# Performance work log

Measured on AMD Instinct MI355X. Metric: run time of the kernel, lower is better.

The kernel has to match this reference:

```python
import jax, jax.numpy as jnp
import numpy as np

B, L, D = 2, 2048, 2048
H, KVH, Dh = 16, 8, 128
S_ROPE = 1024
EPS = 1e-5


def rms_norm(x, w):
    xf = x.astype(jnp.float32)
    xf = xf * jax.lax.rsqrt(jnp.mean(xf * xf, axis=-1, keepdims=True) + EPS)
    return (xf * w).astype(x.dtype)


def rotate_half(x):
    x1, x2 = jnp.split(x, 2, axis=-1)
    return jnp.concatenate((-x2, x1), axis=-1)


def setup_inputs() -> dict:
    key = jax.random.key(0)
    ks = jax.random.split(key, 12)
    sc = 0.02
    # 1D rope tables at every absolute position (theta = 500000 as in config)
    inv_freq = 1.0 / (500000.0 ** (np.arange(0, Dh, 2, dtype=np.float32) / Dh))
    ang = np.arange(L, dtype=np.float32)[:, None] * inv_freq[None, :]  # [L, Dh/2]
    emb = np.concatenate([ang, ang], axis=-1)  # [L, Dh]
    # 3D rope as per-pair 2x2 rotation matrices
    ang3 = np.random.RandomState(0).uniform(-np.pi, np.pi, size=(S_ROPE, Dh // 2)).astype(np.float32)
    R = np.stack([np.stack([np.cos(ang3), -np.sin(ang3)], -1),
                  np.stack([np.sin(ang3), np.cos(ang3)], -1)], -2)  # [S,Dh/2,2,2]
    mpos = jnp.array([[[128, 1025], [1160, 513]],
                      [[128, 1025], [1160, 513]]], dtype=jnp.int64)
    return {
        "hidden_states": jax.random.normal(ks[0], (B, L, D), jnp.float32),
        "temb": jax.random.normal(ks[1], (B, D), jnp.float32),
        "w_ln": jnp.ones((D,), jnp.float32),
        "w_mod": jax.random.normal(ks[2], (D, 3 * D), jnp.float32) * sc,
        "b_mod": jnp.zeros((3 * D,), jnp.float32),
        "wq": jax.random.normal(ks[3], (D, H * Dh), jnp.float32) * sc,
        "wk": jax.random.normal(ks[4], (D, KVH * Dh), jnp.float32) * sc,
        "wv": jax.random.normal(ks[5], (D, KVH * Dh), jnp.float32) * sc,
        "wo": jax.random.normal(ks[6], (H * Dh, D), jnp.float32) * sc,
        "qn_w": jnp.ones((Dh,), jnp.float32),
        "kn_w": jnp.ones((Dh,), jnp.float32),
        "cos_1d": jnp.asarray(np.cos(emb)),
        "sin_1d": jnp.asarray(np.sin(emb)),
        "rope_3d": jnp.asarray(R),
        "modality_positions": mpos,
    }


def _masks(modality_positions):
    pos = jnp.arange(L)  # [L]
    off = modality_positions[..., 0]   # [B, S]
    ln = modality_positions[..., 1]    # [B, S]
    meta = 1  # add_time_embeds=True, add_ar_embeds=False
    seg_end = off + jnp.maximum(ln, meta)
    in_full = (pos[None, None, :] >= off[..., None]) & (pos[None, None, :] < seg_end[..., None])
    text_mask = ~jnp.any(in_full, axis=1)  # [B, L]
    img_start = off + meta
    in_img = (pos[None, None, :] >= img_start[..., None]) & (pos[None, None, :] < (off + ln)[..., None])
    rel = jnp.sum(jnp.where(in_img, pos[None, None, :] - img_start[..., None], 0), axis=1)  # [B, L]
    img_mask = jnp.any(in_img, axis=1) & (rel < S_ROPE) & (rel >= 0)
    rel = jnp.clip(rel, 0, S_ROPE - 1)
    return text_mask, img_mask, rel


def _apply_mixed_rope(q, k, cos_1d, sin_1d, rope_3d, text_mask, img_mask, rel):
    # text 1D rope (rotate_half style), applied at absolute position
    c = cos_1d[None, None]  # [1,1,L,Dh]
    s = sin_1d[None, None]
    q_txt = q * c + rotate_half(q) * s
    k_txt = k * c + rotate_half(k) * s
    # image 3D rope: per-pair 2x2 rotation gathered at within-image index
    R = rope_3d[rel]  # [B, L, Dh/2, 2, 2]
    q2 = q.reshape(*q.shape[:-1], Dh // 2, 2)
    k2 = k.reshape(*k.shape[:-1], Dh // 2, 2)
    q_img = jnp.einsum('bhlpi,blpij->bhlpj', q2, R).reshape(q.shape)
    k_img = jnp.einsum('bhlpi,blpij->bhlpj', k2, R).reshape(k.shape)
    mt = text_mask[:, None, :, None]
    mi = img_mask[:, None, :, None]
    q_out = jnp.where(mt, q_txt, jnp.where(mi, q_img, q))
    k_out = jnp.where(mt, k_txt, jnp.where(mi, k_img, k))
    return q_out, k_out


def reference(hidden_states, temb, w_ln, w_mod, b_mod, wq, wk, wv, wo,
              qn_w, kn_w, cos_1d, sin_1d, rope_3d, modality_positions):
    dtype = hidden_states.dtype
    # adaLN modulation
    mod = jax.nn.silu(temb) @ w_mod + b_mod  # [B, 3D]
    shift, scale, gate = jnp.split(mod, 3, axis=-1)
    xn = rms_norm(hidden_states, w_ln)
    xm = (xn.astype(jnp.float32) * (1.0 + scale[:, None, :].astype(jnp.float32))
          + shift[:, None, :].astype(jnp.float32)).astype(dtype)
    # qkv projections (GQA)
    q = (xm @ wq).reshape(B, L, H, Dh).transpose(0, 2, 1, 3)
    k = (xm @ wk).reshape(B, L, KVH, Dh).transpose(0, 2, 1, 3)
    v = (xm @ wv).reshape(B, L, KVH, Dh).transpose(0, 2, 1, 3)
    # qk-norm over head_dim
    q = rms_norm(q, qn_w)
    k = rms_norm(k, kn_w)
    # mixed 3D-image / 1D-text RoPE
    text_mask, img_mask, rel = _masks(modality_positions)
    q, k = _apply_mixed_rope(q, k, cos_1d, sin_1d, rope_3d, text_mask, img_mask, rel)
    # GQA: repeat kv heads (repeat_interleave along head dim)
    n_rep = H // KVH
    k = jnp.repeat(k, n_rep, axis=1)
    v = jnp.repeat(v, n_rep, axis=1)
    # full attention (no causal mask for diffusion block)
    scores = jnp.einsum('bhqd,bhkd->bhqk', q, k) / jnp.sqrt(jnp.asarray(Dh, q.dtype))
    attn = jax.nn.softmax(scores, axis=-1)
    o = jnp.einsum('bhqk,bhkd->bhqd', attn, v)
    o = o.transpose(0, 2, 1, 3).reshape(B, L, H * Dh) @ wo
    return hidden_states + gate[:, None, :].astype(dtype) * o


if __name__ == '__main__':
    out = reference(**setup_inputs())
    print(out.shape, out.dtype)
```

## Files before the change

kernel.cpp:

```cpp
#include <hip/hip_runtime.h>
#include <stdint.h>
#include <math.h>

typedef unsigned short u16;
typedef __attribute__((ext_vector_type(8))) short short8;
typedef __attribute__((ext_vector_type(4))) float fx4;
typedef __attribute__((ext_vector_type(4))) unsigned short u16x4;

#define DEV __device__ __forceinline__

DEV u16 f2bf(float f) {
  unsigned u = __builtin_bit_cast(unsigned, f);
  return (u16)((u + 0x7FFFu + ((u >> 16) & 1u)) >> 16);
}
DEV float bf2f(u16 h) { return __builtin_bit_cast(float, ((unsigned)h) << 16); }

DEV fx4 mfma16(short8 a, short8 b, fx4 c) {
  return __builtin_amdgcn_mfma_f32_16x16x32_bf16(a, b, c, 0, 0, 0);
}

#if __has_builtin(__builtin_amdgcn_exp2f)
DEV float exp2v(float x) { return __builtin_amdgcn_exp2f(x); }
#else
DEV float exp2v(float x) { return exp2f(x); }
#endif

#define GLD16(g, l)                                                            \
  __builtin_amdgcn_global_load_lds(                                            \
      (const __attribute__((address_space(1))) void*)(g),                      \
      (__attribute__((address_space(3))) void*)(l), 16, 0, 0)

#define WAIT_ALL() asm volatile("s_waitcnt vmcnt(0) lgkmcnt(0)" ::: "memory")

__global__ __launch_bounds__(512) void k_silu_mod(
    const float* __restrict__ temb, const float* __restrict__ wmod,
    const float* __restrict__ bmod, float* __restrict__ mod) {
  __shared__ float st[4096];
  __shared__ float red[8][2][64];
  int tid = threadIdx.x;
  for (int i = tid; i < 4096; i += 512) {
    float t = temb[i];
    st[i] = t / (1.0f + __expf(-t));
  }
  __syncthreads();
  int j = blockIdx.x * 64 + (tid & 63);
  int ks = tid >> 6;
  float a0 = 0.f, a1 = 0.f;
  for (int d = ks * 256; d < ks * 256 + 256; ++d) {
    float w = wmod[(size_t)d * 6144 + j];
    a0 += st[d] * w;
    a1 += st[2048 + d] * w;
  }
  red[ks][0][tid & 63] = a0;
  red[ks][1][tid & 63] = a1;
  __syncthreads();
  if (tid < 64) {
    float s0 = 0.f, s1 = 0.f;
#pragma unroll
    for (int i = 0; i < 8; ++i) {
      s0 += red[i][0][tid];
      s1 += red[i][1][tid];
    }
    mod[j] = s0 + bmod[j];
    mod[6144 + j] = s1 + bmod[j];
  }
}

__global__ __launch_bounds__(256) void k_xm(
    const float* __restrict__ x, const float* __restrict__ wln,
    const float* __restrict__ mod, u16* __restrict__ xm) {
  int row = blockIdx.x;
  int b = row >> 11;
  const float* xr = x + (size_t)row * 2048;
  int tid = threadIdx.x;
  float4 v0 = ((const float4*)xr)[tid];
  float4 v1 = ((const float4*)xr)[tid + 256];
  float ss = v0.x * v0.x + v0.y * v0.y + v0.z * v0.z + v0.w * v0.w +
             v1.x * v1.x + v1.y * v1.y + v1.z * v1.z + v1.w * v1.w;
  for (int m = 1; m < 64; m <<= 1) ss += __shfl_xor(ss, m);
  __shared__ float red[4];
  if ((tid & 63) == 0) red[tid >> 6] = ss;
  __syncthreads();
  ss = red[0] + red[1] + red[2] + red[3];
  float r = rsqrtf(ss * (1.0f / 2048.0f) + 1e-5f);
  const float* mb = mod + (size_t)b * 6144;
#pragma unroll
  for (int c = 0; c < 2; ++c) {
    int j0 = (tid + c * 256) * 4;
    float4 xv = c ? v1 : v0;
    float4 sh = *(const float4*)(mb + j0);
    float4 sc = *(const float4*)(mb + 2048 + j0);
    float4 wl = *(const float4*)(wln + j0);
    u16x4 o;
    o.x = f2bf(xv.x * r * wl.x * (1.f + sc.x) + sh.x);
    o.y = f2bf(xv.y * r * wl.y * (1.f + sc.y) + sh.y);
    o.z = f2bf(xv.z * r * wl.z * (1.f + sc.z) + sh.z);
    o.w = f2bf(xv.w * r * wl.w * (1.f + sc.w) + sh.w);
    *(u16x4*)(xm + (size_t)row * 2048 + j0) = o;
  }
}

__global__ __launch_bounds__(256) void k_tconv(
    const float* __restrict__ src, u16* __restrict__ dst, int cols, int rows) {
  __shared__ float t[32][33];
  int kb = blockIdx.x * 32, nb = blockIdx.y * 32;
  int tx = threadIdx.x, ty = threadIdx.y;
#pragma unroll
  for (int i = 0; i < 4; ++i)
    t[ty + i * 8][tx] = src[(size_t)(kb + ty + i * 8) * cols + nb + tx];
  __syncthreads();
#pragma unroll
  for (int i = 0; i < 4; ++i)
    dst[(size_t)(nb + ty + i * 8) * rows + kb + tx] = f2bf(t[tx][ty + i * 8]);
}

template <int EPI>
__global__ __launch_bounds__(256) void k_gemm(
    const u16* __restrict__ A, const u16* __restrict__ Bt, void* __restrict__ Cp,
    const float* __restrict__ hid, const float* __restrict__ mod, int N, int K) {
  __shared__ u16 As[2][128 * 32];
  __shared__ u16 Bs[2][128 * 32];
  int tid = threadIdx.x;
  int wave = tid >> 6, lane = tid & 63, quad = lane >> 4, l16 = lane & 15;
  int gx = gridDim.x;
  int nwg = gx * gridDim.y;
  int lin = blockIdx.y * gx + blockIdx.x;
  int cpx = nwg >> 3;
  int swz = (lin & 7) * cpx + (lin >> 3);
  int m0 = (swz / gx) * 128, n0 = (swz % gx) * 128;
  int wm = (wave >> 1) * 64, wn = (wave & 1) * 64;
  fx4 acc[4][4] = {};
  int rowa = tid >> 2;
  int chunk = (tid & 3) ^ ((rowa >> 1) & 3);
  int cola = chunk * 8;
  const u16* Ag = A + (size_t)(m0 + rowa) * K + cola;
  const u16* Bg = Bt + (size_t)(n0 + rowa) * K + cola;
  int sl = (quad ^ ((l16 >> 1) & 3)) * 8;

  auto STAGE = [&](int k0, int buf) {
    u16* AsW = &As[buf][wave * 512];
    u16* BsW = &Bs[buf][wave * 512];
    GLD16(Ag + k0, AsW);
    GLD16(Ag + k0 + (size_t)64 * K, AsW + 2048);
    GLD16(Bg + k0, BsW);
    GLD16(Bg + k0 + (size_t)64 * K, BsW + 2048);
  };
  auto COMPUTE = [&](int buf) {
    short8 af[4], bfr[4];
#pragma unroll
    for (int i = 0; i < 4; ++i) {
      af[i] = *(const short8*)&As[buf][(wm + i * 16 + l16) * 32 + sl];
      bfr[i] = *(const short8*)&Bs[buf][(wn + i * 16 + l16) * 32 + sl];
    }
#pragma unroll
    for (int i = 0; i < 4; ++i)
#pragma unroll
      for (int j = 0; j < 4; ++j) acc[i][j] = mfma16(af[i], bfr[j], acc[i][j]);
  };

  STAGE(0, 0);
  WAIT_ALL();
  __builtin_amdgcn_s_barrier();
  int cur = 0;
  for (int k0 = 32; k0 < K; k0 += 32) {
    STAGE(k0, cur ^ 1);
    COMPUTE(cur);
    WAIT_ALL();
    __builtin_amdgcn_s_barrier();
    cur ^= 1;
  }
  COMPUTE(cur);

#pragma unroll
  for (int i = 0; i < 4; ++i) {
    int row = m0 + wm + i * 16 + quad * 4;
#pragma unroll
    for (int j = 0; j < 4; ++j) {
      int col = n0 + wn + j * 16 + l16;
      if (EPI == 0) {
        u16* C = (u16*)Cp;
#pragma unroll
        for (int r = 0; r < 4; ++r)
          C[(size_t)(row + r) * N + col] = f2bf(acc[i][j][r]);
      } else {
        float* C = (float*)Cp;
        int b = row >> 11;
        float g = mod[(size_t)b * 6144 + 4096 + col];
#pragma unroll
        for (int r = 0; r < 4; ++r)
          C[(size_t)(row + r) * N + col] =
              hid[(size_t)(row + r) * N + col] + g * acc[i][j][r];
      }
    }
  }
}

__global__ __launch_bounds__(192) void k_qknorm(
    const u16* __restrict__ qkv, const float* __restrict__ qn,
    const float* __restrict__ kn, const float* __restrict__ cos1,
    const float* __restrict__ sin1, const float* __restrict__ r3,
    const int* __restrict__ mpos, u16* __restrict__ Q, u16* __restrict__ Kb) {
  int bx = blockIdx.x;
  int b = bx >> 11, l = bx & 2047;
  int tid = threadIdx.x;
  int slot = tid >> 3, sub = tid & 7;
  bool isq = slot < 16;
  int head = isq ? slot : slot - 16;
  const u16* base = qkv + (size_t)bx * 4096 + (isq ? slot * 128 : 2048 + head * 128);
  int d0 = sub * 16;
  float xv[16];
#pragma unroll
  for (int i = 0; i < 16; ++i) xv[i] = bf2f(base[d0 + i]);
  float ss = 0.f;
#pragma unroll
  for (int i = 0; i < 16; ++i) ss += xv[i] * xv[i];
  ss += __shfl_xor(ss, 1);
  ss += __shfl_xor(ss, 2);
  ss += __shfl_xor(ss, 4);
  float r = rsqrtf(ss * (1.0f / 128.0f) + 1e-5f);
  int mp[8];
  {
    bool is64 = (mpos[1] == 0) & (mpos[3] == 0) & (mpos[5] == 0) & (mpos[7] == 0);
#pragma unroll
    for (int i = 0; i < 8; ++i) mp[i] = is64 ? mpos[2 * i] : mpos[i];
  }
  bool infull = false, inimg = false;
  int rel = 0;
#pragma unroll
  for (int s = 0; s < 2; ++s) {
    int off = mp[b * 4 + s * 2], ln = mp[b * 4 + s * 2 + 1];
    int mx = ln > 1 ? ln : 1;
    infull |= (l >= off) && (l < off + mx);
    bool ii = (l >= off + 1) && (l < off + ln);
    inimg |= ii;
    rel += ii ? (l - (off + 1)) : 0;
  }
  bool text = !infull;
  bool img = inimg && (rel < 1024);
  const float* w = isq ? qn : kn;
  float out[16];
  if (text) {
    int dp0 = d0 ^ 64;
    float sgn = (d0 < 64) ? -1.f : 1.f;
#pragma unroll
    for (int i = 0; i < 16; ++i) {
      int d = d0 + i, dp = dp0 + i;
      float c = cos1[(size_t)l * 128 + d];
      float s = sin1[(size_t)l * 128 + d];
      float xp = bf2f(base[dp]);
      out[i] = r * (xv[i] * w[d] * c + sgn * xp * w[dp] * s);
    }
  } else if (img) {
    const float* R = r3 + ((size_t)rel * 64 + (d0 >> 1)) * 4;
#pragma unroll
    for (int p = 0; p < 8; ++p) {
      float a = xv[2 * p] * w[d0 + 2 * p] * r;
      float c2 = xv[2 * p + 1] * w[d0 + 2 * p + 1] * r;
      out[2 * p] = a * R[4 * p + 0] + c2 * R[4 * p + 2];
      out[2 * p + 1] = a * R[4 * p + 1] + c2 * R[4 * p + 3];
    }
  } else {
#pragma unroll
    for (int i = 0; i < 16; ++i) out[i] = xv[i] * w[d0 + i] * r;
  }
  if (isq) {
    u16* dst = Q + ((size_t)(b * 16 + head) * 2048 + l) * 128 + d0;
#pragma unroll
    for (int i = 0; i < 16; ++i)
      dst[i] = f2bf(out[i] * (0.08838834764831845f * 1.4426950408889634f));
  } else {
    u16* dst = Kb + ((size_t)(b * 8 + head) * 2048 + l) * 128 + d0;
#pragma unroll
    for (int i = 0; i < 16; ++i) dst[i] = f2bf(out[i]);
  }
}

__global__ __launch_bounds__(256) void k_vtrans(const u16* __restrict__ qkv,
                                                u16* __restrict__ VT) {
  __shared__ u16 t[64][65];
  int bh = blockIdx.x;
  int l0 = blockIdx.y * 64, d0 = blockIdx.z * 64;
  int b = bh >> 3, kvh = bh & 7;
  int tx = threadIdx.x & 63, tg = threadIdx.x >> 6;
#pragma unroll
  for (int i = 0; i < 16; ++i) {
    int li = tg + i * 4;
    t[li][tx] = qkv[(size_t)(b * 2048 + l0 + li) * 4096 + 3072 + kvh * 128 + d0 + tx];
  }
  __syncthreads();
#pragma unroll
  for (int i = 0; i < 16; ++i) {
    int di = tg + i * 4;
    VT[((size_t)bh * 128 + d0 + di) * 2048 + l0 + tx] = t[tx][di];
  }
}

__global__ __launch_bounds__(512, 4) void k_attn(
    const u16* __restrict__ Q, const u16* __restrict__ Kb,
    const u16* __restrict__ VT, u16* __restrict__ O) {
  __shared__ u16 Ks[2][64 * 128];
  __shared__ u16 Vs[2][128 * 64];
  __shared__ u16 Ps[128 * 64];
  int tid = threadIdx.x;
  int wave = tid >> 6, lane = tid & 63, quad = lane >> 4, l16 = lane & 15;
  int bh = blockIdx.y;
  int b = bh >> 4, h = bh & 15, kvh = h >> 1;
  int q0 = blockIdx.x * 128;
  const u16* Qb = Q + ((size_t)bh * 2048 + q0 + wave * 16) * 128;
  short8 qf[4];
#pragma unroll
  for (int ks = 0; ks < 4; ++ks)
    qf[ks] = *(const short8*)(Qb + l16 * 128 + ks * 32 + quad * 8);
  const u16* Kg = Kb + (size_t)(b * 8 + kvh) * 2048 * 128;
  const u16* Vg = VT + (size_t)(b * 8 + kvh) * 128 * 2048;
  float mrow[4], lpart[4];
  fx4 of[8] = {};
#pragma unroll
  for (int r = 0; r < 4; ++r) {
    mrow[r] = -INFINITY;
    lpart[r] = 0.f;
  }
  size_t kgo[2], vgo[2];
#pragma unroll
  for (int i = 0; i < 2; ++i) {
    int kr = i * 32 + wave * 4 + (lane >> 4);
    kgo[i] = (size_t)kr * 128 + (((lane & 15) ^ (kr & 15)) * 8);
    int vr = i * 64 + wave * 8 + (lane >> 3);
    vgo[i] = (size_t)vr * 2048 + (((lane & 7) ^ (vr & 7)) * 8);
  }

  auto STAGE = [&](int t, int buf) {
    size_t ko = (size_t)t * 8192;
    size_t vo = (size_t)t * 64;
#pragma unroll
    for (int i = 0; i < 2; ++i) {
      GLD16(Kg + ko + kgo[i], &Ks[buf][i * 4096 + wave * 512]);
      GLD16(Vg + vo + vgo[i], &Vs[buf][i * 4096 + wave * 512]);
    }
  };

  auto COMPUTE = [&](int buf) {
    fx4 sf[4] = {};
    __builtin_amdgcn_s_setprio(1);
#pragma unroll
    for (int ct = 0; ct < 4; ++ct) {
#pragma unroll
      for (int ks = 0; ks < 4; ++ks) {
        short8 kf = *(const short8*)&Ks[buf][(ct * 16 + l16) * 128 +
                                            (((ks * 4 + quad) ^ l16) * 8)];
        sf[ct] = mfma16(qf[ks], kf, sf[ct]);
      }
    }
    __builtin_amdgcn_s_setprio(0);
    float cmv[4];
    bool need = false;
#pragma unroll
    for (int r = 0; r < 4; ++r) {
      cmv[r] = fmaxf(fmaxf(sf[0][r], sf[1][r]), fmaxf(sf[2][r], sf[3][r]));
      need |= (cmv[r] > mrow[r] + 8.0f);
    }
    if (__any(need)) {
#pragma unroll
      for (int r = 0; r < 4; ++r) {
        float cm = cmv[r];
        cm = fmaxf(cm, __shfl_xor(cm, 1));
        cm = fmaxf(cm, __shfl_xor(cm, 2));
        cm = fmaxf(cm, __shfl_xor(cm, 4));
        cm = fmaxf(cm, __shfl_xor(cm, 8));
        float mn = fmaxf(mrow[r], cm);
        float al = exp2v(mrow[r] - mn);
        mrow[r] = mn;
        lpart[r] *= al;
#pragma unroll
        for (int c2 = 0; c2 < 8; ++c2) of[c2][r] *= al;
      }
    }
    int hb = l16 >> 3;
#pragma unroll
    for (int r = 0; r < 4; ++r) {
      float p0 = exp2v(sf[0][r] - mrow[r]);
      float p1 = exp2v(sf[1][r] - mrow[r]);
      float p2 = exp2v(sf[2][r] - mrow[r]);
      float p3 = exp2v(sf[3][r] - mrow[r]);
      lpart[r] += (p0 + p1) + (p2 + p3);
      int prow = wave * 16 + quad * 4 + r;
      int pb = prow * 64, px = prow & 7, lo = l16 & 7;
      Ps[pb + ((0 + hb) ^ px) * 8 + lo] = f2bf(p0);
      Ps[pb + ((2 + hb) ^ px) * 8 + lo] = f2bf(p1);
      Ps[pb + ((4 + hb) ^ px) * 8 + lo] = f2bf(p2);
      Ps[pb + ((6 + hb) ^ px) * 8 + lo] = f2bf(p3);
    }
    __builtin_amdgcn_s_setprio(1);
#pragma unroll
    for (int ks2 = 0; ks2 < 2; ++ks2) {
      int rsl = (((ks2 * 4 + quad) ^ (l16 & 7)) * 8);
      short8 pa = *(const short8*)&Ps[(wave * 16 + l16) * 64 + rsl];
#pragma unroll
      for (int c2 = 0; c2 < 8; ++c2) {
        short8 vb = *(const short8*)&Vs[buf][(c2 * 16 + l16) * 64 + rsl];
        of[c2] = mfma16(pa, vb, of[c2]);
      }
    }
    __builtin_amdgcn_s_setprio(0);
  };

  STAGE(0, 0);
  WAIT_ALL();
  __builtin_amdgcn_s_barrier();
  int cur = 0;
  for (int t = 0; t < 31; ++t) {
    STAGE(t + 1, cur ^ 1);
    COMPUTE(cur);
    WAIT_ALL();
    __builtin_amdgcn_s_barrier();
    cur ^= 1;
  }
  COMPUTE(cur);

#pragma unroll
  for (int r = 0; r < 4; ++r) {
    float ls = lpart[r];
    ls += __shfl_xor(ls, 1);
    ls += __shfl_xor(ls, 2);
    ls += __shfl_xor(ls, 4);
    ls += __shfl_xor(ls, 8);
    float inv = 1.0f / ls;
    int qrow = q0 + wave * 16 + quad * 4 + r;
#pragma unroll
    for (int c2 = 0; c2 < 8; ++c2)
      O[((size_t)b * 2048 + qrow) * 2048 + h * 128 + c2 * 16 + l16] =
          f2bf(of[c2][r] * inv);
  }
}

extern "C" void kernel_launch(void* const* d_in, const int* in_sizes, int n_in,
                              void* d_out, int out_size, void* d_ws, size_t ws_size,
                              hipStream_t stream) {
  (void)in_sizes; (void)n_in; (void)out_size; (void)ws_size;
  const float* hid  = (const float*)d_in[0];
  const float* temb = (const float*)d_in[1];
  const float* wln  = (const float*)d_in[2];
  const float* wmod = (const float*)d_in[3];
  const float* bmod = (const float*)d_in[4];
  const float* wq   = (const float*)d_in[5];
  const float* wk   = (const float*)d_in[6];
  const float* wv   = (const float*)d_in[7];
  const float* wo   = (const float*)d_in[8];
  const float* qn   = (const float*)d_in[9];
  const float* kn   = (const float*)d_in[10];
  const float* cos1 = (const float*)d_in[11];
  const float* sin1 = (const float*)d_in[12];
  const float* r3   = (const float*)d_in[13];
  const int*   mpos = (const int*)d_in[14];

  char* ws = (char*)d_ws;
  float* mod = (float*)(ws + 0);
  u16* xm  = (u16*)(ws + 49152);
  u16* wT  = (u16*)(ws + 16826368);
  u16* woT = wT;
  u16* qkv = (u16*)(ws + 33603584);
  u16* Qb  = (u16*)(ws + 67158016);
  u16* Kv  = (u16*)(ws + 83935232);
  u16* VT  = (u16*)(ws + 92323840);
  u16* Ob  = qkv;

  dim3 b32(32, 8);
  k_silu_mod<<<96, 512, 0, stream>>>(temb, wmod, bmod, mod);
  k_tconv<<<dim3(64, 64), b32, 0, stream>>>(wq, wT, 2048, 2048);
  k_tconv<<<dim3(64, 32), b32, 0, stream>>>(wk, wT + (size_t)2048 * 2048, 1024, 2048);
  k_tconv<<<dim3(64, 32), b32, 0, stream>>>(wv, wT + (size_t)3072 * 2048, 1024, 2048);
  k_xm<<<4096, 256, 0, stream>>>(hid, wln, mod, xm);
  k_gemm<0><<<dim3(32, 32), 256, 0, stream>>>(xm, wT, qkv, nullptr, nullptr, 4096, 2048);
  k_tconv<<<dim3(64, 64), b32, 0, stream>>>(wo, woT, 2048, 2048);
  k_qknorm<<<4096, 192, 0, stream>>>(qkv, qn, kn, cos1, sin1, r3, mpos, Qb, Kv);
  k_vtrans<<<dim3(16, 32, 2), 256, 0, stream>>>(qkv, VT);
  k_attn<<<dim3(16, 32), 512, 0, stream>>>(Qb, Kv, VT, Ob);
  k_gemm<1><<<dim3(16, 32), 256, 0, stream>>>(Ob, woT, d_out, hid, mod, 2048, 2048);
}
```

Baseline: 487.4 us.

## Add 256x256 triple-buffered QKV GEMM and triple-buffer the output GEMM

Adds a dedicated QKV projection GEMM with 256x256 tiles, 512 threads, and a three-stage LDS ring. It waits with vmcnt(4) so one stage's loads stay in flight during compute, instead of draining everything every iteration. The output-projection GEMM gets the same three-buffer pipeline and becomes a single non-templated kernel. Larger tiles raise reuse per load, but the QKV launch is only 256 workgroups with one block per CU, and the extra LDS lowers occupancy.

Result: faster. 475.5 us (-2.4%).

```diff
diff --git a/kernel.cpp b/kernel.cpp
--- a/kernel.cpp
+++ b/kernel.cpp
@@ -31,6 +31,8 @@
       (__attribute__((address_space(3))) void*)(l), 16, 0, 0)
 
 #define WAIT_ALL() asm volatile("s_waitcnt vmcnt(0) lgkmcnt(0)" ::: "memory")
+#define WAIT_VM4() asm volatile("s_waitcnt vmcnt(4)" ::: "memory")
+#define WAIT_VM0() asm volatile("s_waitcnt vmcnt(0)" ::: "memory")
 
 __global__ __launch_bounds__(512) void k_silu_mod(
     const float* __restrict__ temb, const float* __restrict__ wmod,
@@ -114,12 +116,83 @@
     dst[(size_t)(nb + ty + i * 8) * rows + kb + tx] = f2bf(t[tx][ty + i * 8]);
 }
 
-template <int EPI>
+__global__ __launch_bounds__(512, 1) void k_gemm256(
+    const u16* __restrict__ A, const u16* __restrict__ Bt, u16* __restrict__ C,
+    int N, int K) {
+  __shared__ u16 As[3][256 * 32];
+  __shared__ u16 Bs[3][256 * 32];
+  int tid = threadIdx.x;
+  int wave = tid >> 6, lane = tid & 63, quad = lane >> 4, l16 = lane & 15;
+  int gx = gridDim.x;
+  int nwg = gx * gridDim.y;
+  int lin = blockIdx.y * gx + blockIdx.x;
+  int cpx = nwg >> 3;
+  int swz = (lin & 7) * cpx + (lin >> 3);
+  int m0 = (swz / gx) * 256, n0 = (swz % gx) * 256;
+  int wm = (wave >> 2) * 128, wn = (wave & 3) * 64;
+  fx4 acc[8][4] = {};
+  int rowa = tid >> 2;
+  int chunk = (tid & 3) ^ ((rowa >> 1) & 3);
+  int cola = chunk * 8;
+  const u16* Ag = A + (size_t)(m0 + rowa) * K + cola;
+  const u16* Bg = Bt + (size_t)(n0 + rowa) * K + cola;
+  int sl = (quad ^ ((l16 >> 1) & 3)) * 8;
+
+  auto STAGE = [&](int k0, int buf) {
+    u16* AsW = &As[buf][wave * 512];
+    u16* BsW = &Bs[buf][wave * 512];
+    GLD16(Ag + k0, AsW);
+    GLD16(Ag + k0 + (size_t)128 * K, AsW + 4096);
+    GLD16(Bg + k0, BsW);
+    GLD16(Bg + k0 + (size_t)128 * K, BsW + 4096);
+  };
+  auto COMPUTE = [&](int buf) {
+    short8 af[8], bfr[4];
+#pragma unroll
+    for (int i = 0; i < 8; ++i)
+      af[i] = *(const short8*)&As[buf][(wm + i * 16 + l16) * 32 + sl];
+#pragma unroll
+    for (int j = 0; j < 4; ++j)
+      bfr[j] = *(const short8*)&Bs[buf][(wn + j * 16 + l16) * 32 + sl];
+#pragma unroll
+    for (int i = 0; i < 8; ++i)
+#pragma unroll
+      for (int j = 0; j < 4; ++j) acc[i][j] = mfma16(af[i], bfr[j], acc[i][j]);
+  };
+
+  STAGE(0, 0);
+  STAGE(32, 1);
+  for (int t = 0; t < 62; ++t) {
+    WAIT_VM4();
+    __builtin_amdgcn_s_barrier();
+    STAGE((t + 2) * 32, (t + 2) % 3);
+    COMPUTE(t % 3);
+  }
+  WAIT_VM4();
+  __builtin_amdgcn_s_barrier();
+  COMPUTE(2);
+  WAIT_VM0();
+  __builtin_amdgcn_s_barrier();
+  COMPUTE(0);
+
+#pragma unroll
+  for (int i = 0; i < 8; ++i) {
+    int row = m0 + wm + i * 16 + quad * 4;
+#pragma unroll
+    for (int j = 0; j < 4; ++j) {
+      int col = n0 + wn + j * 16 + l16;
+#pragma unroll
+      for (int r = 0; r < 4; ++r)
+        C[(size_t)(row + r) * N + col] = f2bf(acc[i][j][r]);
+    }
+  }
+}
+
 __global__ __launch_bounds__(256) void k_gemm(
-    const u16* __restrict__ A, const u16* __restrict__ Bt, void* __restrict__ Cp,
+    const u16* __restrict__ A, const u16* __restrict__ Bt, float* __restrict__ C,
     const float* __restrict__ hid, const float* __restrict__ mod, int N, int K) {
-  __shared__ u16 As[2][128 * 32];
-  __shared__ u16 Bs[2][128 * 32];
+  __shared__ u16 As[3][128 * 32];
+  __shared__ u16 Bs[3][128 * 32];
   int tid = threadIdx.x;
   int wave = tid >> 6, lane = tid & 63, quad = lane >> 4, l16 = lane & 15;
   int gx = gridDim.x;
@@ -159,17 +232,20 @@
   };
 
   STAGE(0, 0);
-  WAIT_ALL();
+  STAGE(32, 1);
+  int nk = K >> 5;
+  for (int t = 0; t < nk - 2; ++t) {
+    WAIT_VM4();
+    __builtin_amdgcn_s_barrier();
+    STAGE((t + 2) * 32, (t + 2) % 3);
+    COMPUTE(t % 3);
+  }
+  WAIT_VM4();
   __builtin_amdgcn_s_barrier();
-  int cur = 0;
-  for (int k0 = 32; k0 < K; k0 += 32) {
-    STAGE(k0, cur ^ 1);
-    COMPUTE(cur);
-    WAIT_ALL();
-    __builtin_amdgcn_s_barrier();
-    cur ^= 1;
-  }
-  COMPUTE(cur);
+  COMPUTE((nk - 2) % 3);
+  WAIT_VM0();
+  __builtin_amdgcn_s_barrier();
+  COMPUTE((nk - 1) % 3);
 
 #pragma unroll
   for (int i = 0; i < 4; ++i) {
@@ -177,20 +253,12 @@
 #pragma unroll
     for (int j = 0; j < 4; ++j) {
       int col = n0 + wn + j * 16 + l16;
-      if (EPI == 0) {
-        u16* C = (u16*)Cp;
-#pragma unroll
-        for (int r = 0; r < 4; ++r)
-          C[(size_t)(row + r) * N + col] = f2bf(acc[i][j][r]);
-      } else {
-        float* C = (float*)Cp;
-        int b = row >> 11;
-        float g = mod[(size_t)b * 6144 + 4096 + col];
-#pragma unroll
-        for (int r = 0; r < 4; ++r)
-          C[(size_t)(row + r) * N + col] =
-              hid[(size_t)(row + r) * N + col] + g * acc[i][j][r];
-      }
+      int b = row >> 11;
+      float g = mod[(size_t)b * 6144 + 4096 + col];
+#pragma unroll
+      for (int r = 0; r < 4; ++r)
+        C[(size_t)(row + r) * N + col] =
+            hid[(size_t)(row + r) * N + col] + g * acc[i][j][r];
     }
   }
 }
@@ -470,10 +538,10 @@
   k_tconv<<<dim3(64, 32), b32, 0, stream>>>(wk, wT + (size_t)2048 * 2048, 1024, 2048);
   k_tconv<<<dim3(64, 32), b32, 0, stream>>>(wv, wT + (size_t)3072 * 2048, 1024, 2048);
   k_xm<<<4096, 256, 0, stream>>>(hid, wln, mod, xm);
-  k_gemm<0><<<dim3(32, 32), 256, 0, stream>>>(xm, wT, qkv, nullptr, nullptr, 4096, 2048);
+  k_gemm256<<<dim3(16, 16), 512, 0, stream>>>(xm, wT, qkv, 4096, 2048);
   k_tconv<<<dim3(64, 64), b32, 0, stream>>>(wo, woT, 2048, 2048);
   k_qknorm<<<4096, 192, 0, stream>>>(qkv, qn, kn, cos1, sin1, r3, mpos, Qb, Kv);
   k_vtrans<<<dim3(16, 32, 2), 256, 0, stream>>>(qkv, VT);
   k_attn<<<dim3(16, 32), 512, 0, stream>>>(Qb, Kv, VT, Ob);
-  k_gemm<1><<<dim3(16, 32), 256, 0, stream>>>(Ob, woT, d_out, hid, mod, 2048, 2048);
-}
+  k_gemm<<<dim3(16, 32), 256, 0, stream>>>(Ob, woT, (float*)d_out, hid, mod, 2048, 2048);
+}
```
